# Kernel tuning notes

Hardware: AMD Instinct MI355X
Metric: run time of the kernel (lower is better)

Reference implementation:

```python
import jax, jax.numpy as jnp
import numpy as np

B, S, D = 1, 2048, 2048
H = 16
HD = D // H           # 128
FFN_H = 5632          # int(2*4*D/3) rounded up to multiple of 256
EPS = 1e-5
ROPE_THETA = 10000.0


def rms_norm(x, w, eps=EPS):
    # x * rsqrt(mean(x^2, -1) + eps) * w
    return x * jax.lax.rsqrt(jnp.mean(x * x, axis=-1, keepdims=True) + eps) * w


def apply_rope(x, cos, sin):
    # x: [B, S, H, HD]; cos/sin: [S, HD//2]
    b, s, h, hd = x.shape
    xr = x.reshape(b, s, h, hd // 2, 2)
    x_re, x_im = xr[..., 0], xr[..., 1]
    c = cos[None, :, None, :]
    sn = sin[None, :, None, :]
    o_re = x_re * c - x_im * sn
    o_im = x_re * sn + x_im * c
    return jnp.stack([o_re, o_im], axis=-1).reshape(b, s, h, hd)


def setup_inputs() -> dict:
    key = jax.random.key(0)
    ks = jax.random.split(key, 10)
    x = jax.random.normal(ks[0], (B, S, D), dtype=jnp.float32)
    # RoPE frequencies (Llama-style)
    inv_freq = 1.0 / (ROPE_THETA ** (np.arange(0, HD, 2, dtype=np.float32) / HD))
    angles = np.outer(np.arange(S, dtype=np.float32), inv_freq)  # [S, HD//2]
    freqs_cos = jnp.asarray(np.cos(angles), dtype=jnp.float32)
    freqs_sin = jnp.asarray(np.sin(angles), dtype=jnp.float32)
    # causal mask: 1 = keep, 0 = masked
    mask = jnp.tril(jnp.ones((S, S), dtype=jnp.int32))[None, None]
    sc = 0.02
    return {
        "x": x,
        "freqs_cos": freqs_cos,
        "freqs_sin": freqs_sin,
        "mask": mask,
        "wq": jax.random.normal(ks[1], (D, D), jnp.float32) * sc,
        "wk": jax.random.normal(ks[2], (D, D), jnp.float32) * sc,
        "wv": jax.random.normal(ks[3], (D, D), jnp.float32) * sc,
        "wo": jax.random.normal(ks[4], (D, D), jnp.float32) * sc,
        "w1": jax.random.normal(ks[5], (D, FFN_H), jnp.float32) * sc,
        "w2": jax.random.normal(ks[6], (FFN_H, D), jnp.float32) * sc,
        "w3": jax.random.normal(ks[7], (D, FFN_H), jnp.float32) * sc,
        "attn_norm_w": jnp.ones((D,), jnp.float32),
        "ffn_norm_w": jnp.ones((D,), jnp.float32),
    }


def reference(x, freqs_cos, freqs_sin, mask, wq, wk, wv, wo, w1, w2, w3,
              attn_norm_w, ffn_norm_w):
    b, s, d = x.shape
    # --- attention block ---
    xn = rms_norm(x, attn_norm_w)
    q = (xn @ wq).reshape(b, s, H, HD)
    k = (xn @ wk).reshape(b, s, H, HD)
    v = (xn @ wv).reshape(b, s, H, HD)
    q = apply_rope(q, freqs_cos, freqs_sin)
    k = apply_rope(k, freqs_cos, freqs_sin)
    scores = jnp.einsum('bqhd,bkhd->bhqk', q, k) / jnp.sqrt(jnp.float32(HD))
    scores = jnp.where(mask == 0, -jnp.inf, scores)
    probs = jax.nn.softmax(scores, axis=-1)
    attn = jnp.einsum('bhqk,bkhd->bqhd', probs, v).reshape(b, s, d)
    h = x + attn @ wo
    # --- SwiGLU FFN block ---
    hn = rms_norm(h, ffn_norm_w)
    ff = (jax.nn.silu(hn @ w1) * (hn @ w3)) @ w2
    return h + ff
```

## Files before the change

### kernel.cpp

```cpp
#include <hip/hip_runtime.h>
#include <hip/hip_bf16.h>

typedef __bf16 bf16x8 __attribute__((ext_vector_type(8)));
typedef float f32x4 __attribute__((ext_vector_type(4)));
typedef unsigned short u16x8 __attribute__((ext_vector_type(8)));
typedef unsigned short u16x4 __attribute__((ext_vector_type(4)));

#define DEV static __device__ __forceinline__

DEV unsigned short f2bf(float f) {
    unsigned u = __builtin_bit_cast(unsigned, f);
    u += 0x7fffu + ((u >> 16) & 1u);
    return (unsigned short)(u >> 16);
}
DEV float bf2f(unsigned short h) {
    unsigned u = ((unsigned)h) << 16;
    return __builtin_bit_cast(float, u);
}

DEV void gl2lds16(const void* g, void* l) {
    __builtin_amdgcn_global_load_lds(
        (const __attribute__((address_space(1))) void*)g,
        (__attribute__((address_space(3))) void*)l, 16, 0, 0);
}

#define WAITV(N) asm volatile("s_waitcnt vmcnt(" #N ")" ::: "memory")
#define SBAR()   asm volatile("s_barrier" ::: "memory")

#define STAGE128D(KT, BUF)                                                    \
    _Pragma("unroll")                                                         \
    for (int sl = 0; sl < 3; ++sl) {                                          \
        const unsigned short* sbase = (sl == 0)                               \
            ? A  + (size_t)bm * K                                             \
            : BT + (size_t)(bn + (sl - 1) * 128) * K;                         \
        _Pragma("unroll")                                                     \
        for (int j = 0; j < 2; ++j) {                                         \
            const unsigned short* g = sbase + (size_t)(srow + j * 64) * K     \
                                      + koff + (KT) * 64 + lc;                \
            gl2lds16(g, &lds[BUF][sl][wave * 512 + j * 4096]);                \
        }                                                                     \
    }

#define DSREAD128(BUF)                                                        \
    {                                                                         \
        const char* Ab = (const char*)&lds[BUF][0][0];                        \
        const char* Bb = (const char*)&lds[BUF][1 + (wn >> 1)][0];            \
        _Pragma("unroll")                                                     \
        for (int m4 = 0; m4 < 4; ++m4)                                        \
            _Pragma("unroll")                                                 \
            for (int kk = 0; kk < 2; ++kk)                                    \
                a_[m4][kk] = *(const bf16x8*)(Ab +                            \
                    (wm * 64 + m4 * 16 + lr) * 128 +                          \
                    ((kk * 64 + lg * 16) ^ xsw));                             \
        _Pragma("unroll")                                                     \
        for (int n2 = 0; n2 < 4; ++n2)                                        \
            _Pragma("unroll")                                                 \
            for (int kk = 0; kk < 2; ++kk)                                    \
                b_[n2][kk] = *(const bf16x8*)(Bb +                            \
                    ((wn & 1) * 64 + n2 * 16 + lr) * 128 +                    \
                    ((kk * 64 + lg * 16) ^ xsw));                             \
    }

#define MFMA128                                                               \
    __builtin_amdgcn_s_setprio(1);                                            \
    _Pragma("unroll")                                                         \
    for (int m4 = 0; m4 < 4; ++m4)                                            \
        _Pragma("unroll")                                                     \
        for (int n2 = 0; n2 < 4; ++n2)                                        \
            _Pragma("unroll")                                                 \
            for (int kk = 0; kk < 2; ++kk)                                    \
                acc[m4][n2] = __builtin_amdgcn_mfma_f32_16x16x32_bf16(        \
                    a_[m4][kk], b_[n2][kk], acc[m4][n2], 0, 0, 0);            \
    __builtin_amdgcn_s_setprio(0);

template <int EPI>
__global__ __launch_bounds__(512, 2)
void gemm128d(const unsigned short* __restrict__ A,
              const unsigned short* __restrict__ BT,
              unsigned short* __restrict__ outB,
              float* __restrict__ outP,
              int M, int N, int K,
              const float* __restrict__ cs, const float* __restrict__ sn,
              unsigned short* __restrict__ vT)
{
    __shared__ alignas(16) unsigned short lds[3][3][8192];
    const int tid  = threadIdx.x;
    const int lane = tid & 63;
    const int wave = tid >> 6;
    const int wm = wave >> 2;
    const int wn = wave & 3;
    const int lr = lane & 15;
    const int lg = lane >> 4;
    const int gy  = gridDim.y;
    const int lin = blockIdx.y * gridDim.x + blockIdx.x;
    const int cpx = (gridDim.x * gy) >> 3;
    const int swz = (lin & 7) * cpx + (lin >> 3);
    const int bm = (swz % gy) * 128;
    const int bn = (swz / gy) * 256;
    const int xsw  = (lr & 7) << 4;
    const int srow = tid >> 3;
    const int lc   = ((tid & 7) ^ (srow & 7)) * 8;
    int koff, NT;
    if constexpr (EPI == 1 || EPI == 3) {
        const int Kh = K >> 1; koff = blockIdx.z * Kh; NT = Kh >> 6;
    } else {
        koff = 0; NT = K >> 6;
    }

    f32x4 acc[4][4] = {};
    bf16x8 a_[4][2], b_[4][2];

    STAGE128D(0, 0);
    STAGE128D(1, 1);
    WAITV(6); SBAR();
    DSREAD128(0);

    int bc = 0;
    for (int kt = 0; kt < NT - 2; ++kt) {
        const int nb = (bc == 0) ? 2 : bc - 1;
        STAGE128D(kt + 2, nb);
        MFMA128;
        WAITV(6); SBAR();
        const int rb = (bc == 2) ? 0 : bc + 1;
        DSREAD128(rb);
        bc = rb;
    }
    MFMA128;
    WAITV(0); SBAR();
    {
        const int rb = (bc == 2) ? 0 : bc + 1;
        DSREAD128(rb);
    }
    MFMA128;

#pragma unroll
    for (int m4 = 0; m4 < 4; ++m4) {
        const int row = bm + wm * 64 + m4 * 16 + lg * 4;
#pragma unroll
        for (int n2 = 0; n2 < 4; ++n2) {
            const int col = bn + wn * 64 + n2 * 16 + lr;
            if constexpr (EPI == 4) {
                if (bn >= 4096) {
                    u16x4 o;
#pragma unroll
                    for (int r = 0; r < 4; ++r) o[r] = f2bf(acc[m4][n2][r]);
                    *(u16x4*)(vT + (size_t)(col - 4096) * 2048 + row) = o;
                } else {
#pragma unroll
                    for (int r = 0; r < 4; ++r) {
                        const float v  = acc[m4][n2][r];
                        const float vo = __shfl_xor(v, 1);
                        const int rr = row + r;
                        const int i0 = (col & 127) >> 1;
                        const float c = cs[rr * 64 + i0];
                        const float s = sn[rr * 64 + i0];
                        const float o = (lr & 1) ? (vo * s + v * c)
                                                 : (v * c - vo * s);
                        outB[(size_t)rr * N + col] = f2bf(o);
                    }
                }
            } else {
#pragma unroll
                for (int r = 0; r < 4; ++r) {
                    if constexpr (EPI == 1) {
                        outP[(size_t)blockIdx.z * M * N + (size_t)(row + r) * N + col] = acc[m4][n2][r];
                    } else if constexpr (EPI == 3) {
                        unsafeAtomicAdd(&outP[(size_t)(row + r) * N + col], acc[m4][n2][r]);
                    } else {
                        const float v  = acc[m4][n2][r];
                        const float vo = __shfl_xor(v, 1);
                        const float x1 = (lr & 1) ? vo : v;
                        const float x3 = (lr & 1) ? v : vo;
                        const float g  = x1 / (1.0f + __expf(-x1)) * x3;
                        if (!(lr & 1))
                            outB[(size_t)(row + r) * (N >> 1) + (col >> 1)] = f2bf(g);
                    }
                }
            }
        }
    }
}

__global__ __launch_bounds__(256)
void reduce2_norm(const float* __restrict__ res, const float* __restrict__ p,
                  const float* __restrict__ w, float* __restrict__ hout,
                  unsigned short* __restrict__ nout)
{
    const int row = blockIdx.x, tid = threadIdx.x;
    const float4* r4 = (const float4*)(res + (size_t)row * 2048);
    const float4* a4 = (const float4*)(p   + (size_t)row * 2048);
    const float4* b4 = (const float4*)(p + (size_t)2048 * 2048 + (size_t)row * 2048);
    float4* h4 = (float4*)(hout + (size_t)row * 2048);
    float4 h[2];
    float ss = 0.f;
#pragma unroll
    for (int i = 0; i < 2; ++i) {
        const int idx = i * 256 + tid;
        const float4 r = r4[idx], a = a4[idx], b = b4[idx];
        float4 v = make_float4(r.x + a.x + b.x, r.y + a.y + b.y,
                               r.z + a.z + b.z, r.w + a.w + b.w);
        h[i] = v; h4[idx] = v;
        ss += v.x * v.x + v.y * v.y + v.z * v.z + v.w * v.w;
    }
#pragma unroll
    for (int off = 32; off; off >>= 1) ss += __shfl_xor(ss, off);
    __shared__ float red[4];
    if ((tid & 63) == 0) red[tid >> 6] = ss;
    __syncthreads();
    const float tot = red[0] + red[1] + red[2] + red[3];
    const float sc = rsqrtf(tot * (1.0f / 2048.0f) + 1e-5f);
#pragma unroll
    for (int i = 0; i < 2; ++i) {
        const int idx = i * 256 + tid;
        const float4 wv = ((const float4*)w)[idx];
        u16x4 o;
        o[0] = f2bf(h[i].x * sc * wv.x); o[1] = f2bf(h[i].y * sc * wv.y);
        o[2] = f2bf(h[i].z * sc * wv.z); o[3] = f2bf(h[i].w * sc * wv.w);
        *(u16x4*)(nout + (size_t)row * 2048 + idx * 4) = o;
    }
}

__global__ __launch_bounds__(256)
void rmsnorm_kernel(const float* __restrict__ x, const float* __restrict__ w,
                    unsigned short* __restrict__ out)
{
    const int row = blockIdx.x;
    const int tid = threadIdx.x;
    const float* xr = x + (size_t)row * 2048;
    const float4 a = *reinterpret_cast<const float4*>(xr + tid * 8);
    const float4 b = *reinterpret_cast<const float4*>(xr + tid * 8 + 4);
    float ss = a.x * a.x + a.y * a.y + a.z * a.z + a.w * a.w
             + b.x * b.x + b.y * b.y + b.z * b.z + b.w * b.w;
#pragma unroll
    for (int off = 32; off; off >>= 1) ss += __shfl_xor(ss, off);
    __shared__ float red[4];
    if ((tid & 63) == 0) red[tid >> 6] = ss;
    __syncthreads();
    const float tot = red[0] + red[1] + red[2] + red[3];
    const float sc = rsqrtf(tot * (1.0f / 2048.0f) + 1e-5f);
    const float4 wa = *reinterpret_cast<const float4*>(w + tid * 8);
    const float4 wb = *reinterpret_cast<const float4*>(w + tid * 8 + 4);
    u16x8 o;
    o[0] = f2bf(a.x * sc * wa.x); o[1] = f2bf(a.y * sc * wa.y);
    o[2] = f2bf(a.z * sc * wa.z); o[3] = f2bf(a.w * sc * wa.w);
    o[4] = f2bf(b.x * sc * wb.x); o[5] = f2bf(b.y * sc * wb.y);
    o[6] = f2bf(b.z * sc * wb.z); o[7] = f2bf(b.w * sc * wb.w);
    *reinterpret_cast<u16x8*>(out + (size_t)row * 2048 + tid * 8) = o;
}

DEV void convT_half(const float* __restrict__ w, unsigned short* __restrict__ wT,
                    int K, int N, int rmul, int radd, int bk, int bn,
                    int tid, unsigned short (*t)[66])
{
    const int r = tid >> 4, c4 = (tid & 15) * 4;
#pragma unroll
    for (int i = 0; i < 4; ++i) {
        const int row = r + i * 16;
        const float4 v = *reinterpret_cast<const float4*>(w + (size_t)(bk + row) * N + bn + c4);
        t[row][c4 + 0] = f2bf(v.x); t[row][c4 + 1] = f2bf(v.y);
        t[row][c4 + 2] = f2bf(v.z); t[row][c4 + 3] = f2bf(v.w);
    }
    __syncthreads();
#pragma unroll
    for (int i = 0; i < 4; ++i) {
        const int n = r + i * 16;
        u16x4 o;
#pragma unroll
        for (int e = 0; e < 4; ++e) o[e] = t[c4 + e][n];
        *reinterpret_cast<u16x4*>(wT + (size_t)(rmul * (bn + n) + radd) * K + bk + c4) = o;
    }
}

__global__ __launch_bounds__(256)
void convT3_kernel(const float* __restrict__ w0, const float* __restrict__ w1,
                   const float* __restrict__ w2v, unsigned short* __restrict__ wT)
{
    __shared__ unsigned short t[64][66];
    const int z = blockIdx.z;
    const float* w = (z == 0) ? w0 : (z == 1) ? w1 : w2v;
    convT_half(w, wT + (size_t)z * 2048 * 2048, 2048, 2048, 1, 0,
               blockIdx.y * 64, blockIdx.x * 64, threadIdx.x, t);
}

DEV void ct_decode(int t2,
                   const float* wo, const float* w1, const float* w3,
                   const float* w2,
                   unsigned short* woT, unsigned short* w13T, unsigned short* w2T,
                   const float*& w, unsigned short*& wT,
                   int& K, int& N, int& rmul, int& radd, int& bk, int& bn)
{
    if (t2 < 1024) {
        w = wo; wT = woT; K = 2048; N = 2048; rmul = 1; radd = 0;
        bk = (t2 >> 5) * 64; bn = (t2 & 31) * 64;
    } else if (t2 < 6656) {
        const int u = t2 - 1024;
        const int z = u / 2816, rm = u % 2816;
        w = z ? w3 : w1; wT = w13T; K = 2048; N = 5632; rmul = 2; radd = z;
        bk = (rm / 88) * 64; bn = (rm % 88) * 64;
    } else {
        const int u = t2 - 6656;
        w = w2; wT = w2T; K = 5632; N = 2048; rmul = 1; radd = 0;
        bk = (u / 32) * 64; bn = (u % 32) * 64;
    }
}

__global__ __launch_bounds__(512, 4)
void flash_mega(const unsigned short* __restrict__ q,
                const unsigned short* __restrict__ k,
                const unsigned short* __restrict__ vT,
                unsigned short* __restrict__ attn,
                const float* __restrict__ wo, const float* __restrict__ w1,
                const float* __restrict__ w3, const float* __restrict__ w2,
                unsigned short* __restrict__ woT,
                unsigned short* __restrict__ w13T,
                unsigned short* __restrict__ w2T)
{
    __shared__ alignas(16) unsigned short Ks[2][64][136];
    __shared__ alignas(16) unsigned short Vs[128][72];
    __shared__ alignas(16) unsigned short Ps[8][16][72];

    const int bid = blockIdx.x;
    const int tid = threadIdx.x;

    if (bid >= 256) {
        const int half = tid >> 8;
        const int t256 = tid & 255;
        const int gid  = (bid - 256) * 2 + half;
        const int r = t256 >> 4, c4 = (t256 & 15) * 4;
        unsigned short (*tb)[66] =
            (unsigned short (*)[66])(&Ks[0][0][0] + half * 64 * 66);
        const int TOT = 9472;

        float4 cur[4], nxt[4];
        const float* wC; unsigned short* wTC;
        int KC, NC, rmC, raC, bkC, bnC;
        int t2 = gid;
        bool act = (t2 < TOT);
        if (act) {
            ct_decode(t2, wo, w1, w3, w2, woT, w13T, w2T,
                      wC, wTC, KC, NC, rmC, raC, bkC, bnC);
#pragma unroll
            for (int i = 0; i < 4; ++i)
                cur[i] = *(const float4*)(wC + (size_t)(bkC + r + i * 16) * NC + bnC + c4);
        }
#pragma unroll 1
        for (int it = 0; it < 10; ++it) {
            const int t2n = t2 + 1024;
            const bool actn = (t2n < TOT);
            const float* wN; unsigned short* wTN;
            int KN, NN, rmN, raN, bkN, bnN;
            if (actn) {
                ct_decode(t2n, wo, w1, w3, w2, woT, w13T, w2T,
                          wN, wTN, KN, NN, rmN, raN, bkN, bnN);
#pragma unroll
                for (int i = 0; i < 4; ++i)
                    nxt[i] = *(const float4*)(wN + (size_t)(bkN + r + i * 16) * NN + bnN + c4);
            }
            if (act) {
#pragma unroll
                for (int i = 0; i < 4; ++i) {
                    const int row = r + i * 16;
                    tb[row][c4 + 0] = f2bf(cur[i].x);
                    tb[row][c4 + 1] = f2bf(cur[i].y);
                    tb[row][c4 + 2] = f2bf(cur[i].z);
                    tb[row][c4 + 3] = f2bf(cur[i].w);
                }
            }
            __syncthreads();
            if (act) {
#pragma unroll
                for (int i = 0; i < 4; ++i) {
                    const int n = r + i * 16;
                    u16x4 o;
#pragma unroll
                    for (int e = 0; e < 4; ++e) o[e] = tb[c4 + e][n];
                    *reinterpret_cast<u16x4*>(
                        wTC + (size_t)(rmC * (bnC + n) + raC) * KC + bkC + c4) = o;
                }
            }
            __syncthreads();
            t2 = t2n; act = actn;
            if (actn) {
                wC = wN; wTC = wTN; KC = KN; NC = NN;
                rmC = rmN; raC = raN; bkC = bkN; bnC = bnN;
#pragma unroll
                for (int i = 0; i < 4; ++i) cur[i] = nxt[i];
            }
        }
        return;
    }

    const int hh = bid >> 4;
    const int pi = bid & 15;
    const int lane = tid & 63, wave = tid >> 6;
    const int qt = (wave >> 2) ? (31 - pi) : pi;
    const int lr = lane & 15, lg = lane >> 4;
    const int q0 = qt * 64 + (wave & 3) * 16;
    const int myNT = qt + 1;
    const int NT   = 32 - pi;

    const int kr0 = tid >> 4, kc0 = (tid & 15) * 8;
    const int vr0 = tid >> 3, vc0 = (tid & 7) * 8;

    bf16x8 qf[4];
#pragma unroll
    for (int c = 0; c < 4; ++c)
        qf[c] = *reinterpret_cast<const bf16x8*>(
            q + (size_t)(q0 + lr) * 6144 + hh * 128 + c * 32 + lg * 8);

    f32x4 oacc[8] = {};
    float m_r[4], l_r[4];
#pragma unroll
    for (int r = 0; r < 4; ++r) { m_r[r] = -INFINITY; l_r[r] = 0.0f; }
    const float scale = 0.08838834764831845f;

    u16x8 kreg0, kreg1, vreg0, vreg1;
    auto gload = [&](int kt) {
        const int kv0 = kt * 64;
        kreg0 = *reinterpret_cast<const u16x8*>(k + (size_t)(kv0 + kr0) * 6144 + hh * 128 + kc0);
        kreg1 = *reinterpret_cast<const u16x8*>(k + (size_t)(kv0 + kr0 + 32) * 6144 + hh * 128 + kc0);
        vreg0 = *reinterpret_cast<const u16x8*>(vT + (size_t)(hh * 128 + vr0) * 2048 + kv0 + vc0);
        vreg1 = *reinterpret_cast<const u16x8*>(vT + (size_t)(hh * 128 + vr0 + 64) * 2048 + kv0 + vc0);
    };
    auto lwriteK = [&](int buf) {
        *reinterpret_cast<u16x8*>(&Ks[buf][kr0][kc0])      = kreg0;
        *reinterpret_cast<u16x8*>(&Ks[buf][kr0 + 32][kc0]) = kreg1;
    };
    auto lwriteV = [&]() {
        *reinterpret_cast<u16x8*>(&Vs[vr0][vc0])      = vreg0;
        *reinterpret_cast<u16x8*>(&Vs[vr0 + 64][vc0]) = vreg1;
    };

    gload(0);
    lwriteK(0);
    lwriteV();
    __syncthreads();

    for (int kt = 0; kt < NT; ++kt) {
        const int buf = kt & 1;
        if (kt + 1 < NT) gload(kt + 1);

        if (kt < myNT) {
            const int kv0 = kt * 64;
            const bool masked = (kt == myNT - 1);
            f32x4 s[4] = {};
            __builtin_amdgcn_s_setprio(1);
#pragma unroll
            for (int ct = 0; ct < 4; ++ct)
#pragma unroll
                for (int c = 0; c < 4; ++c) {
                    const bf16x8 kf = *reinterpret_cast<const bf16x8*>(
                        &Ks[buf][ct * 16 + lr][c * 32 + lg * 8]);
                    s[ct] = __builtin_amdgcn_mfma_f32_16x16x32_bf16(qf[c], kf, s[ct], 0, 0, 0);
                }
            __builtin_amdgcn_s_setprio(0);
#pragma unroll
            for (int ct = 0; ct < 4; ++ct)
#pragma unroll
                for (int r = 0; r < 4; ++r) {
                    float v = s[ct][r] * scale;
                    if (masked) {
                        const int kvg = kv0 + ct * 16 + lr;
                        const int qg  = q0 + lg * 4 + r;
                        if (kvg > qg) v = -INFINITY;
                    }
                    s[ct][r] = v;
                }
            float mn[4], alpha[4], rs[4];
#pragma unroll
            for (int r = 0; r < 4; ++r) {
                float v = fmaxf(fmaxf(s[0][r], s[1][r]), fmaxf(s[2][r], s[3][r]));
                v = fmaxf(v, __shfl_xor(v, 1));
                v = fmaxf(v, __shfl_xor(v, 2));
                v = fmaxf(v, __shfl_xor(v, 4));
                v = fmaxf(v, __shfl_xor(v, 8));
                mn[r] = fmaxf(m_r[r], v);
                alpha[r] = __expf(m_r[r] - mn[r]);
                m_r[r] = mn[r];
                rs[r] = 0.0f;
            }
#pragma unroll
            for (int ct = 0; ct < 4; ++ct)
#pragma unroll
                for (int r = 0; r < 4; ++r) {
                    const float p = __expf(s[ct][r] - mn[r]);
                    s[ct][r] = p;
                    rs[r] += p;
                }
#pragma unroll
            for (int r = 0; r < 4; ++r) {
                float t2 = rs[r];
                t2 += __shfl_xor(t2, 1);
                t2 += __shfl_xor(t2, 2);
                t2 += __shfl_xor(t2, 4);
                t2 += __shfl_xor(t2, 8);
                l_r[r] = l_r[r] * alpha[r] + t2;
            }
#pragma unroll
            for (int ot = 0; ot < 8; ++ot)
#pragma unroll
                for (int r = 0; r < 4; ++r) oacc[ot][r] *= alpha[r];

#pragma unroll
            for (int ct = 0; ct < 4; ++ct)
#pragma unroll
                for (int r = 0; r < 4; ++r)
                    Ps[wave][lg * 4 + r][ct * 16 + lr] = f2bf(s[ct][r]);

            __builtin_amdgcn_s_setprio(1);
#pragma unroll
            for (int c2 = 0; c2 < 2; ++c2) {
                const bf16x8 pf = *reinterpret_cast<const bf16x8*>(
                    &Ps[wave][lr][c2 * 32 + lg * 8]);
#pragma unroll
                for (int ot = 0; ot < 8; ++ot) {
                    const bf16x8 vf = *reinterpret_cast<const bf16x8*>(
                        &Vs[ot * 16 + lr][c2 * 32 + lg * 8]);
                    oacc[ot] = __builtin_amdgcn_mfma_f32_16x16x32_bf16(pf, vf, oacc[ot], 0, 0, 0);
                }
            }
            __builtin_amdgcn_s_setprio(0);
        }

        if (kt + 1 < NT) lwriteK(buf ^ 1);
        __syncthreads();
        if (kt + 1 < NT) lwriteV();
        __syncthreads();
    }

#pragma unroll
    for (int ot = 0; ot < 8; ++ot)
#pragma unroll
        for (int r = 0; r < 4; ++r) {
            const float v = oacc[ot][r] / l_r[r];
            attn[(size_t)(q0 + lg * 4 + r) * 2048 + hh * 128 + ot * 16 + lr] = f2bf(v);
        }
}

extern "C" void kernel_launch(void* const* d_in, const int* in_sizes, int n_in,
                              void* d_out, int out_size, void* d_ws, size_t ws_size,
                              hipStream_t stream)
{
    const float* x    = (const float*)d_in[0];
    const float* fcos = (const float*)d_in[1];
    const float* fsin = (const float*)d_in[2];
    const float* wq  = (const float*)d_in[4];
    const float* wk  = (const float*)d_in[5];
    const float* wv  = (const float*)d_in[6];
    const float* wo  = (const float*)d_in[7];
    const float* w1  = (const float*)d_in[8];
    const float* w2  = (const float*)d_in[9];
    const float* w3  = (const float*)d_in[10];
    const float* anw = (const float*)d_in[11];
    const float* fnw = (const float*)d_in[12];
    float* out = (float*)d_out;

    char* ws = (char*)d_ws;
    size_t off = 0;
    auto alloc = [&](size_t bytes) { void* p = ws + off; off += bytes; return p; };
    const size_t SZ_DD = (size_t)2048 * 2048 * 2;
    const size_t SZ_DF = (size_t)2048 * 5632 * 2;

    unsigned short* qkvoT = (unsigned short*)alloc(4 * SZ_DD);
    unsigned short* w13T  = (unsigned short*)alloc(2 * SZ_DF);
    unsigned short* w2T   = (unsigned short*)alloc(SZ_DF);

    char* reg1 = (char*)alloc((size_t)48 * 1024 * 1024);
    unsigned short* xn   = (unsigned short*)reg1;
    unsigned short* qkv  = (unsigned short*)(reg1 + SZ_DD);
    unsigned short* vTb  = (unsigned short*)(reg1 + SZ_DD + 3 * SZ_DD);
    unsigned short* ab   = (unsigned short*)(reg1 + SZ_DD + 4 * SZ_DD);
    float*          pk   = (float*)reg1;
    unsigned short* hn   = (unsigned short*)(reg1 + 4 * SZ_DD);

    char* reg2 = (char*)alloc(SZ_DF);
    unsigned short* t1 = (unsigned short*)reg2;

    convT3_kernel<<<dim3(32, 32, 3), 256, 0, stream>>>(wq, wk, wv, qkvoT);

    rmsnorm_kernel<<<2048, 256, 0, stream>>>(x, anw, xn);
    gemm128d<4><<<dim3(24, 16), 512, 0, stream>>>(xn, qkvoT, qkv, nullptr,
                                                  2048, 6144, 2048, fcos, fsin, vTb);
    flash_mega<<<768, 512, 0, stream>>>(qkv, qkv + 2048, vTb, ab,
                                        wo, w1, w3, w2,
                                        qkvoT + 3 * (size_t)2048 * 2048, w13T, w2T);
    gemm128d<1><<<dim3(8, 16, 2), 512, 0, stream>>>(ab, qkvoT + 3 * (size_t)2048 * 2048,
                                                    nullptr, pk, 2048, 2048, 2048,
                                                    nullptr, nullptr, nullptr);
    reduce2_norm<<<2048, 256, 0, stream>>>(x, pk, fnw, out, hn);

    gemm128d<2><<<dim3(44, 16), 512, 0, stream>>>(hn, w13T, t1, nullptr,
                                                  2048, 11264, 2048,
                                                  nullptr, nullptr, nullptr);
    gemm128d<3><<<dim3(8, 16, 2), 512, 0, stream>>>(t1, w2T, nullptr, out,
                                                    2048, 2048, 5632,
                                                    nullptr, nullptr, nullptr);
}
```

Measured before the change: 402.1 us.

## Merge weight transpose with RMSNorm launch and add lazy softmax rescaling

```diff
diff --git a/kernel.cpp b/kernel.cpp
--- a/kernel.cpp
+++ b/kernel.cpp
@@ -220,12 +220,50 @@
     }
 }
 
+DEV void convT_half(const float* __restrict__ w, unsigned short* __restrict__ wT,
+                    int K, int N, int rmul, int radd, int bk, int bn,
+                    int tid, unsigned short (*t)[66])
+{
+    const int r = tid >> 4, c4 = (tid & 15) * 4;
+#pragma unroll
+    for (int i = 0; i < 4; ++i) {
+        const int row = r + i * 16;
+        const float4 v = *reinterpret_cast<const float4*>(w + (size_t)(bk + row) * N + bn + c4);
+        t[row][c4 + 0] = f2bf(v.x); t[row][c4 + 1] = f2bf(v.y);
+        t[row][c4 + 2] = f2bf(v.z); t[row][c4 + 3] = f2bf(v.w);
+    }
+    __syncthreads();
+#pragma unroll
+    for (int i = 0; i < 4; ++i) {
+        const int n = r + i * 16;
+        u16x4 o;
+#pragma unroll
+        for (int e = 0; e < 4; ++e) o[e] = t[c4 + e][n];
+        *reinterpret_cast<u16x4*>(wT + (size_t)(rmul * (bn + n) + radd) * K + bk + c4) = o;
+    }
+}
+
 __global__ __launch_bounds__(256)
-void rmsnorm_kernel(const float* __restrict__ x, const float* __restrict__ w,
-                    unsigned short* __restrict__ out)
+void prep_kernel(const float* __restrict__ x, const float* __restrict__ anw,
+                 unsigned short* __restrict__ xn,
+                 const float* __restrict__ wq, const float* __restrict__ wk,
+                 const float* __restrict__ wv, unsigned short* __restrict__ qkvoT)
 {
-    const int row = blockIdx.x;
-    const int tid = threadIdx.x;
+    __shared__ unsigned short t[64][66];
+    const int bid = blockIdx.x, tid = threadIdx.x;
+
+    if (bid >= 2048) {
+        const int u = bid - 2048;
+        const int z = u >> 10;
+        const int idx = u & 1023;
+        const float* w = (z == 0) ? wq : (z == 1) ? wk : wv;
+        convT_half(w, qkvoT + (size_t)z * 2048 * 2048, 2048, 2048, 1, 0,
+                   (idx >> 5) * 64, (idx & 31) * 64, tid, t);
+        return;
+    }
+
+    float* red = (float*)&t[0][0];
+    const int row = bid;
     const float* xr = x + (size_t)row * 2048;
     const float4 a = *reinterpret_cast<const float4*>(xr + tid * 8);
     const float4 b = *reinterpret_cast<const float4*>(xr + tid * 8 + 4);
@@ -233,53 +271,18 @@
              + b.x * b.x + b.y * b.y + b.z * b.z + b.w * b.w;
 #pragma unroll
     for (int off = 32; off; off >>= 1) ss += __shfl_xor(ss, off);
-    __shared__ float red[4];
     if ((tid & 63) == 0) red[tid >> 6] = ss;
     __syncthreads();
     const float tot = red[0] + red[1] + red[2] + red[3];
     const float sc = rsqrtf(tot * (1.0f / 2048.0f) + 1e-5f);
-    const float4 wa = *reinterpret_cast<const float4*>(w + tid * 8);
-    const float4 wb = *reinterpret_cast<const float4*>(w + tid * 8 + 4);
+    const float4 wa = *reinterpret_cast<const float4*>(anw + tid * 8);
+    const float4 wb = *reinterpret_cast<const float4*>(anw + tid * 8 + 4);
     u16x8 o;
     o[0] = f2bf(a.x * sc * wa.x); o[1] = f2bf(a.y * sc * wa.y);
     o[2] = f2bf(a.z * sc * wa.z); o[3] = f2bf(a.w * sc * wa.w);
     o[4] = f2bf(b.x * sc * wb.x); o[5] = f2bf(b.y * sc * wb.y);
     o[6] = f2bf(b.z * sc * wb.z); o[7] = f2bf(b.w * sc * wb.w);
-    *reinterpret_cast<u16x8*>(out + (size_t)row * 2048 + tid * 8) = o;
-}
-
-DEV void convT_half(const float* __restrict__ w, unsigned short* __restrict__ wT,
-                    int K, int N, int rmul, int radd, int bk, int bn,
-                    int tid, unsigned short (*t)[66])
-{
-    const int r = tid >> 4, c4 = (tid & 15) * 4;
-#pragma unroll
-    for (int i = 0; i < 4; ++i) {
-        const int row = r + i * 16;
-        const float4 v = *reinterpret_cast<const float4*>(w + (size_t)(bk + row) * N + bn + c4);
-        t[row][c4 + 0] = f2bf(v.x); t[row][c4 + 1] = f2bf(v.y);
-        t[row][c4 + 2] = f2bf(v.z); t[row][c4 + 3] = f2bf(v.w);
-    }
-    __syncthreads();
-#pragma unroll
-    for (int i = 0; i < 4; ++i) {
-        const int n = r + i * 16;
-        u16x4 o;
-#pragma unroll
-        for (int e = 0; e < 4; ++e) o[e] = t[c4 + e][n];
-        *reinterpret_cast<u16x4*>(wT + (size_t)(rmul * (bn + n) + radd) * K + bk + c4) = o;
-    }
-}
-
-__global__ __launch_bounds__(256)
-void convT3_kernel(const float* __restrict__ w0, const float* __restrict__ w1,
-                   const float* __restrict__ w2v, unsigned short* __restrict__ wT)
-{
-    __shared__ unsigned short t[64][66];
-    const int z = blockIdx.z;
-    const float* w = (z == 0) ? w0 : (z == 1) ? w1 : w2v;
-    convT_half(w, wT + (size_t)z * 2048 * 2048, 2048, 2048, 1, 0,
-               blockIdx.y * 64, blockIdx.x * 64, threadIdx.x, t);
+    *reinterpret_cast<u16x8*>(xn + (size_t)row * 2048 + tid * 8) = o;
 }
 
 DEV void ct_decode(int t2,
@@ -466,7 +469,7 @@
                     }
                     s[ct][r] = v;
                 }
-            float mn[4], alpha[4], rs[4];
+            float pmax[4];
 #pragma unroll
             for (int r = 0; r < 4; ++r) {
                 float v = fmaxf(fmaxf(s[0][r], s[1][r]), fmaxf(s[2][r], s[3][r]));
@@ -474,16 +477,28 @@
                 v = fmaxf(v, __shfl_xor(v, 2));
                 v = fmaxf(v, __shfl_xor(v, 4));
                 v = fmaxf(v, __shfl_xor(v, 8));
-                mn[r] = fmaxf(m_r[r], v);
-                alpha[r] = __expf(m_r[r] - mn[r]);
-                m_r[r] = mn[r];
-                rs[r] = 0.0f;
-            }
+                pmax[r] = v;
+            }
+            bool small = true;
+#pragma unroll
+            for (int r = 0; r < 4; ++r) small = small && (pmax[r] - m_r[r] <= 8.0f);
+            if (!__all(small)) {
+#pragma unroll
+                for (int r = 0; r < 4; ++r) {
+                    const float mn = fmaxf(m_r[r], pmax[r]);
+                    const float alpha = __expf(m_r[r] - mn);
+                    m_r[r] = mn;
+                    l_r[r] *= alpha;
+#pragma unroll
+                    for (int ot = 0; ot < 8; ++ot) oacc[ot][r] *= alpha;
+                }
+            }
+            float rs[4] = {0.f, 0.f, 0.f, 0.f};
 #pragma unroll
             for (int ct = 0; ct < 4; ++ct)
 #pragma unroll
                 for (int r = 0; r < 4; ++r) {
-                    const float p = __expf(s[ct][r] - mn[r]);
+                    const float p = __expf(s[ct][r] - m_r[r]);
                     s[ct][r] = p;
                     rs[r] += p;
                 }
@@ -494,12 +509,8 @@
                 t2 += __shfl_xor(t2, 2);
                 t2 += __shfl_xor(t2, 4);
                 t2 += __shfl_xor(t2, 8);
-                l_r[r] = l_r[r] * alpha[r] + t2;
-            }
-#pragma unroll
-            for (int ot = 0; ot < 8; ++ot)
-#pragma unroll
-                for (int r = 0; r < 4; ++r) oacc[ot][r] *= alpha[r];
+                l_r[r] += t2;
+            }
 
 #pragma unroll
             for (int ct = 0; ct < 4; ++ct)
@@ -576,9 +587,8 @@
     char* reg2 = (char*)alloc(SZ_DF);
     unsigned short* t1 = (unsigned short*)reg2;
 
-    convT3_kernel<<<dim3(32, 32, 3), 256, 0, stream>>>(wq, wk, wv, qkvoT);
-
-    rmsnorm_kernel<<<2048, 256, 0, stream>>>(x, anw, xn);
+    prep_kernel<<<5120, 256, 0, stream>>>(x, anw, xn, wq, wk, wv, qkvoT);
+
     gemm128d<4><<<dim3(24, 16), 512, 0, stream>>>(xn, qkvoT, qkv, nullptr,
                                                   2048, 6144, 2048, fcos, fsin, vTb);
     flash_mega<<<768, 512, 0, stream>>>(qkv, qkv + 2048, vTb, ab,
```

New measurement: 401.6 us (median of 3 runs). Within noise of the previous version (-0.1%).
